# Performance work log

Hardware: AMD Instinct MI355X
Metric: run time of the kernel (lower is better)

Reference implementation:

```python
import jax, jax.numpy as jnp
import numpy as np

B, L, TOPK, NUM_RBF, NUM_POS, MAX_REL, CH = 4, 1024, 30, 16, 16, 32, 128
EDGE_IN = NUM_POS + NUM_RBF * 25 + 18  # 434
NODE_IN = 22


def _normalize(x, axis=-1):
    n = jnp.linalg.norm(x, axis=axis, keepdims=True)
    return jnp.where(n > 0, x / jnp.where(n > 0, n, 1.0), 0.0)


def layer_norm(x, g, b, eps=1e-5):
    mu = jnp.mean(x, axis=-1, keepdims=True)
    var = jnp.var(x, axis=-1, keepdims=True)
    return (x - mu) / jnp.sqrt(var + eps) * g + b


def gather_nodes_d(nodes, idx):
    # nodes [B,M,C], idx [B,N,K] -> [B,N,K,C]
    Bn, N, K = idx.shape
    out = jnp.take_along_axis(nodes, idx.reshape(Bn, N * K, 1), axis=1)
    return out.reshape(Bn, N, K, nodes.shape[-1])


def gather_edges(edges, idx):
    # edges [B,N,N,C], idx [B,N,K] -> [B,N,K,C]
    return jnp.take_along_axis(edges, idx[..., None], axis=2)


def cal_dihedral(Xf, eps=1e-7):
    U = _normalize(Xf[:, 1:, :] - Xf[:, :-1, :])
    u_0, u_1, u_2 = U[:, :-2], U[:, 1:-1], U[:, 2:]
    n_0 = _normalize(jnp.cross(u_0, u_1))
    n_1 = _normalize(jnp.cross(u_1, u_2))
    cosD = jnp.clip(jnp.sum(n_0 * n_1, -1), -1 + eps, 1 - eps)
    v = _normalize(jnp.cross(n_0, n_1))
    return jnp.sign(jnp.sum(-v * u_1, -1)) * jnp.arccos(cosD)


def _dihedrals(X, eps=1e-7):
    Bn, N = X.shape[0], X.shape[1]
    Xf = X[:, :, :3, :].reshape(Bn, 3 * N, 3)
    D = jnp.pad(cal_dihedral(Xf), ((0, 0), (1, 2))).reshape(Bn, N, 3)
    dihedral_feats = jnp.concatenate([jnp.cos(D), jnp.sin(D)], -1)
    U = _normalize(Xf[:, 1:, :] - Xf[:, :-1, :])
    cosA = jnp.clip(jnp.sum(U[:, :-2] * U[:, 1:-1], -1), -1 + eps, 1 - eps)
    A = jnp.pad(jnp.arccos(cosA), ((0, 0), (1, 2))).reshape(Bn, N, 3)
    angle_feats = jnp.concatenate([jnp.cos(A), jnp.sin(A)], -1)
    return jnp.concatenate([dihedral_feats, angle_feats], -1)  # [B,N,12]


def _quaternions(R):
    diag = jnp.diagonal(R, axis1=-2, axis2=-1)
    Rxx, Ryy, Rzz = diag[..., 0], diag[..., 1], diag[..., 2]
    mags = 0.5 * jnp.sqrt(jnp.abs(1.0 + jnp.stack([Rxx - Ryy - Rzz, -Rxx + Ryy - Rzz, -Rxx - Ryy + Rzz], -1)))
    signs = jnp.sign(jnp.stack([R[..., 2, 1] - R[..., 1, 2], R[..., 0, 2] - R[..., 2, 0], R[..., 1, 0] - R[..., 0, 1]], -1))
    w = jnp.sqrt(jax.nn.relu(1.0 + jnp.sum(diag, -1, keepdims=True))) / 2.0
    return _normalize(jnp.concatenate([signs * mags, w], -1))


def _orientations_coarse_gl_tuple(X, E_idx):
    V = X  # [B,N,4,3]
    Bn, N = X.shape[0], X.shape[1]
    Xf = X[:, :, :3, :].reshape(Bn, 3 * N, 3)
    U = _normalize(Xf[:, 1:, :] - Xf[:, :-1, :])
    u_0, u_1 = U[:, :-2], U[:, 1:-1]
    n_0 = _normalize(jnp.cross(u_0, u_1))[:, ::3]  # [B,N-1,3]
    b_1 = _normalize(u_0 - u_1)[:, ::3]
    Xa = Xf[:, ::3]  # N-atom coords [B,N,3]
    Q = jnp.stack([b_1, n_0, jnp.cross(b_1, n_0)], 2).reshape(Bn, N - 1, 9)
    Q = jnp.pad(Q, ((0, 0), (0, 1), (0, 0)))  # [B,N,9]
    Qm = Q.reshape(Bn, N, 3, 3)
    Q_neighbors = gather_nodes_d(Q, E_idx).reshape(Bn, N, -1, 3, 3)
    X_nb = gather_nodes_d(V[:, :, 1, :], E_idx)
    N_nb = gather_nodes_d(V[:, :, 0, :], E_idx)
    C_nb = gather_nodes_d(V[:, :, 2, :], E_idx)
    O_nb = gather_nodes_d(V[:, :, 3, :], E_idx)
    dXn = jnp.stack([X_nb, N_nb, C_nb, O_nb], 3) - Xa[:, :, None, None, :]  # [B,N,K,4,3]
    dU = jnp.einsum('bnij,bnkaj->bnkai', Qm, dXn)
    Kn = E_idx.shape[-1]
    E_direct = _normalize(dU).reshape(Bn, N, Kn, 12)
    R = jnp.einsum('bnji,bnkjl->bnkil', Qm, Q_neighbors)
    q = _quaternions(R)  # [B,N,K,4]
    dX_inner = V[:, :, jnp.array([0, 2, 3]), :] - Xa[:, :, None, :]
    V_direct = _normalize(jnp.einsum('bnij,bnaj->bnai', Qm, dX_inner)).reshape(Bn, N, 9)
    return V_direct, E_direct, q


def _dist(Xc, mask, eps=1e-6):
    mask_2D = mask[:, None, :] * mask[:, :, None]
    D = mask_2D * jnp.sqrt(jnp.sum((Xc[:, None, :, :] - Xc[:, :, None, :]) ** 2, -1) + eps)
    D_max = jnp.max(D, -1, keepdims=True)
    D_adjust = D + (1.0 - mask_2D) * D_max
    negD, E_idx = jax.lax.top_k(-D_adjust, min(TOPK, Xc.shape[1]))
    return -negD, E_idx


def _dist_seq(res_idx):
    D = jnp.abs(res_idx[:, :, None] - res_idx[:, None, :])
    _, E_idx = jax.lax.top_k(-D, min(TOPK, res_idx.shape[1]))
    return E_idx


def _rbf(D):
    D_mu = jnp.linspace(2.0, 22.0, NUM_RBF)
    D_sigma = (22.0 - 2.0) / NUM_RBF
    return jnp.exp(-(((D[..., None] - D_mu) / D_sigma) ** 2))


def _get_rbf(A, Bm, E_idx):
    D = jnp.sqrt(jnp.sum((A[:, :, None, :] - Bm[:, None, :, :]) ** 2, -1) + 1e-6)
    return _rbf(gather_edges(D[..., None], E_idx)[..., 0])


PAIRS = [('N', 'N'), ('C', 'C'), ('O', 'O'), ('Cb', 'Cb'), ('Ca', 'N'), ('Ca', 'C'), ('Ca', 'O'), ('Ca', 'Cb'),
         ('N', 'C'), ('N', 'O'), ('N', 'Cb'), ('Cb', 'C'), ('Cb', 'O'), ('O', 'C'), ('N', 'Ca'), ('C', 'Ca'),
         ('O', 'Ca'), ('Cb', 'Ca'), ('C', 'N'), ('O', 'N'), ('Cb', 'N'), ('C', 'Cb'), ('O', 'Cb'), ('C', 'O')]


def _forward(X, mask, residue_idx, chain_labels, W_pos, b_pos, W_edge, W_node, g_edge, b_edge, g_node, b_node):
    bvec = X[:, :, 1, :] - X[:, :, 0, :]
    cvec = X[:, :, 2, :] - X[:, :, 1, :]
    avec = jnp.cross(bvec, cvec)
    Cb = -0.58273431 * avec + 0.56802827 * bvec - 0.54067466 * cvec + X[:, :, 1, :]
    atoms = {'N': X[:, :, 0, :], 'Ca': X[:, :, 1, :], 'C': X[:, :, 2, :], 'O': X[:, :, 3, :], 'Cb': Cb}
    D_neighbors, E_idx = _dist(atoms['Ca'], mask)
    E_idx_res = _dist_seq(residue_idx)
    E_idx = jnp.where(mask[:, :, None] == 0, E_idx_res, E_idx)
    RBF_all = [_rbf(D_neighbors)]
    for pa, pb in PAIRS:
        RBF_all.append(_get_rbf(atoms[pa], atoms[pb], E_idx))
    RBF_all = jnp.concatenate(RBF_all, -1)  # [B,L,K,400]
    V_angles = _dihedrals(X) * mask[..., None]
    V_direct, E_direct, E_angles = _orientations_coarse_gl_tuple(X, E_idx)
    V_direct = V_direct * mask[..., None]
    offset = residue_idx[:, :, None] - residue_idx[:, None, :]
    E_offset = gather_edges(offset[..., None], E_idx)[..., 0]
    d_chains = (chain_labels[:, :, None] == chain_labels[:, None, :]).astype(jnp.int32)
    E_chains = gather_edges(d_chains[..., None], E_idx)[..., 0]
    d = jnp.clip(E_offset + MAX_REL, 0, 2 * MAX_REL) * E_chains + (1 - E_chains) * (2 * MAX_REL + 1)
    E_positional = jax.nn.one_hot(d, 2 * MAX_REL + 2, dtype=W_pos.dtype) @ W_pos + b_pos
    mask_j = gather_nodes_d(mask[..., None], E_idx)[..., 0]
    fdt = E_direct.dtype
    E = jnp.concatenate([E_positional, RBF_all, E_direct, E_angles,
                         E_chains[..., None].astype(fdt), mask_j[..., None]], -1)  # [B,L,K,434]
    E = layer_norm(E @ W_edge, g_edge, b_edge)
    Vn = jnp.concatenate([V_angles, V_direct, mask[..., None]], -1)  # [B,L,22]
    Vn = layer_norm(Vn @ W_node, g_node, b_node)
    return Vn, E, E_idx


def setup_inputs():
    key = jax.random.key(0)
    ks = jax.random.split(key, 8)
    X = 3.0 * jax.random.normal(ks[0], (B, L, 4, 3), jnp.float32)
    mask = jnp.ones((B, L), jnp.float32)
    residue_idx = jnp.tile(jnp.arange(L, dtype=jnp.int32), (B, 1))
    chain_labels = jax.random.randint(ks[1], (B, L), 0, 2, dtype=jnp.int32)
    s = lambda k, sh: jax.random.normal(k, sh, jnp.float32) * 0.05
    W_pos = s(ks[2], (2 * MAX_REL + 2, NUM_POS))
    b_pos = jnp.zeros((NUM_POS,), jnp.float32)
    W_edge = s(ks[3], (EDGE_IN, CH))
    W_node = s(ks[4], (NODE_IN, CH))
    return dict(X=X, mask=mask, residue_idx=residue_idx, chain_labels=chain_labels,
                W_pos=W_pos, b_pos=b_pos, W_edge=W_edge, W_node=W_node,
                g_edge=jnp.ones((CH,), jnp.float32), b_edge=jnp.zeros((CH,), jnp.float32),
                g_node=jnp.ones((CH,), jnp.float32), b_node=jnp.zeros((CH,), jnp.float32))


def reference(X, mask, residue_idx, chain_labels, W_pos, b_pos, W_edge, W_node, g_edge, b_edge, g_node, b_node):
    return _forward(X, mask, residue_idx, chain_labels, W_pos, b_pos, W_edge, W_node,
                    g_edge, b_edge, g_node, b_node)
```

## Files before the change

kernel.cpp:

```cpp
#include <hip/hip_runtime.h>

#define BATCH 4
#define LEN   1024
#define KNB   30
#define CH    128
#define EIN   434
#define KP    448
#define KST   14
#define ASTR  456
#define CSTR  132
#define AJS   20

typedef unsigned short ushort_t;
typedef __attribute__((ext_vector_type(8))) short bf16x8;
typedef __attribute__((ext_vector_type(4))) float f32x4;

__constant__ int c_pa[24] = {0,2,3,4,1,1,1,1,0,0,0,4,4,3,0,2,3,4,2,3,4,2,3,2};
__constant__ int c_pb[24] = {0,2,3,4,0,2,3,4,2,3,4,2,3,2,1,1,1,1,0,0,0,4,4,3};

struct F3 { float x, y, z; };
__device__ __forceinline__ F3 f3sub(F3 a, F3 b){ return {a.x-b.x, a.y-b.y, a.z-b.z}; }
__device__ __forceinline__ F3 f3cross(F3 a, F3 b){
  return {a.y*b.z - a.z*b.y, a.z*b.x - a.x*b.z, a.x*b.y - a.y*b.x};
}
__device__ __forceinline__ float f3dot(F3 a, F3 b){ return a.x*b.x + a.y*b.y + a.z*b.z; }
__device__ __forceinline__ F3 f3norm(F3 a){
  float s2 = f3dot(a,a);
  float inv = (s2 > 0.f) ? __builtin_amdgcn_rsqf(s2) : 0.f;
  return {a.x*inv, a.y*inv, a.z*inv};
}
__device__ __forceinline__ float fsign(float x){ return (x > 0.f) ? 1.f : ((x < 0.f) ? -1.f : 0.f); }
__device__ __forceinline__ float clip1(float c){ return fminf(fmaxf(c, -1.f + 1e-7f), 1.f - 1e-7f); }

__device__ __forceinline__ void dihedral_cs(F3 ua, F3 ub, F3 uc, float& c, float& s){
  F3 n0 = f3norm(f3cross(ua, ub));
  F3 n1 = f3norm(f3cross(ub, uc));
  float cd = clip1(f3dot(n0, n1));
  F3 v = f3norm(f3cross(n0, n1));
  c = cd;
  s = fsign(-f3dot(v, ub)) * sqrtf(1.f - cd*cd);
}

__device__ __forceinline__ ushort_t f2bf(float f){
  unsigned u = __float_as_uint(f);
  unsigned r = u + 0x7FFFu + ((u >> 16) & 1u);
  return (ushort_t)(r >> 16);
}

__device__ __forceinline__ unsigned cvt_pk(float a, float b){
  unsigned r;
  asm("v_cvt_pk_bf16_f32 %0, %1, %2" : "=v"(r) : "v"(a), "v"(b));
  return r;
}

__device__ __forceinline__ int corig(int c){
  if (c < 16 || c >= 416) return c;
  int base = (c < 216) ? 16 : 216;
  int p = (c - base) >> 3, m = (c - base) & 7;
  return 16 + p*16 + m + ((c < 216) ? 0 : 8);
}

#define DPP_MIN_STEP(v, ctrl) do{                                            \
    unsigned t_ = (unsigned)__builtin_amdgcn_update_dpp(                     \
        (int)0xFFFFFFFF, (int)(v), (ctrl), 0xF, 0xF, false);                 \
    (v) = t_ < (v) ? t_ : (v);                                               \
  } while(0)
__device__ __forceinline__ unsigned wave_min_u32(unsigned v){
  DPP_MIN_STEP(v, 0x111);
  DPP_MIN_STEP(v, 0x112);
  DPP_MIN_STEP(v, 0x114);
  DPP_MIN_STEP(v, 0x118);
  DPP_MIN_STEP(v, 0x142);
  DPP_MIN_STEP(v, 0x143);
  return (unsigned)__builtin_amdgcn_readlane((int)v, 63);
}

__global__ __launch_bounds__(256) void prep_kernel(
    const float* __restrict__ X, const float* __restrict__ mask,
    const float* __restrict__ We,
    float* __restrict__ wCb, float* __restrict__ wQ, float* __restrict__ wVn,
    float* __restrict__ wCa, ushort_t* __restrict__ Wfrag)
{
  if (blockIdx.x >= 16){
    int f = (blockIdx.x - 16)*256 + threadIdx.x;
    if (f >= 8*KST*64) return;
    int t = f / (KST*64);
    int s = (f / 64) % KST;
    int l = f & 63;
    int n  = t*16 + (l & 15);
    int k0 = s*32 + (l >> 4)*8;
    ushort_t v[8];
    #pragma unroll
    for (int j = 0; j < 8; ++j){
      int k = k0 + j;
      v[j] = (k < EIN) ? f2bf(We[(size_t)corig(k)*CH + n]) : (ushort_t)0;
    }
    ulong2* dst = (ulong2*)(Wfrag + (size_t)f*8);
    *dst = *(ulong2*)v;
    return;
  }

  int idx = blockIdx.x * 256 + threadIdx.x;
  int n = idx & (LEN - 1);
  const float* p = X + (size_t)idx * 12;
  const float4* p4 = (const float4*)p;
  float4 q0 = p4[0], q1 = p4[1], q2 = p4[2];
  F3 Na = {q0.x, q0.y, q0.z};
  F3 Ca = {q0.w, q1.x, q1.y};
  F3 Cc = {q1.z, q1.w, q2.x};
  F3 Oa = {q2.y, q2.z, q2.w};
  ((float4*)wCa)[idx] = make_float4(Ca.x, Ca.y, Ca.z, 0.f);
  F3 bv = f3sub(Ca, Na);
  F3 cv = f3sub(Cc, Ca);
  F3 av = f3cross(bv, cv);
  ((float4*)wCb)[idx] = make_float4(
    -0.58273431f*av.x + 0.56802827f*bv.x - 0.54067466f*cv.x + Ca.x,
    -0.58273431f*av.y + 0.56802827f*bv.y - 0.54067466f*cv.y + Ca.y,
    -0.58273431f*av.z + 0.56802827f*bv.z - 0.54067466f*cv.z + Ca.z, 0.f);

  F3 u0 = f3norm(bv);
  F3 u1 = f3norm(cv);

  float Q[9];
  if (n < LEN - 1){
    F3 b1 = f3norm(f3sub(u0, u1));
    F3 n0 = f3norm(f3cross(u0, u1));
    F3 r2 = f3cross(b1, n0);
    Q[0]=b1.x; Q[1]=b1.y; Q[2]=b1.z;
    Q[3]=n0.x; Q[4]=n0.y; Q[5]=n0.z;
    Q[6]=r2.x; Q[7]=r2.y; Q[8]=r2.z;
  } else {
    #pragma unroll
    for (int t = 0; t < 9; ++t) Q[t] = 0.f;
  }
  float4* wq4 = (float4*)(wQ + (size_t)idx*12);
  wq4[0] = make_float4(Q[0], Q[1], Q[2], Q[3]);
  wq4[1] = make_float4(Q[4], Q[5], Q[6], Q[7]);
  wq4[2] = make_float4(Q[8], 0.f, 0.f, 0.f);

  float m = mask[idx];
  bool hp = (n > 0), hn = (n < LEN - 1);
  F3 um1 = {0,0,0}, u2 = {0,0,0}, u3 = {0,0,0};
  if (hp){
    const float* pp = p - 12;
    F3 Cp = {pp[6], pp[7], pp[8]};
    um1 = f3norm(f3sub(Na, Cp));
  }
  if (hn){
    const float* pn = p + 12;
    F3 Nn  = {pn[0], pn[1], pn[2]};
    F3 Can = {pn[3], pn[4], pn[5]};
    u2 = f3norm(f3sub(Nn, Cc));
    u3 = f3norm(f3sub(Can, Nn));
  }
  float cD0=1.f,sD0=0.f, cD1=1.f,sD1=0.f, cD2=1.f,sD2=0.f;
  float cA0=1.f,sA0=0.f, cA1=1.f,sA1=0.f, cA2=1.f,sA2=0.f;
  if (hp){
    dihedral_cs(um1, u0, u1, cD0, sD0);
    cA0 = clip1(f3dot(um1, u0)); sA0 = sqrtf(1.f - cA0*cA0);
  }
  if (hn){
    dihedral_cs(u0, u1, u2, cD1, sD1);
    dihedral_cs(u1, u2, u3, cD2, sD2);
    cA1 = clip1(f3dot(u0, u1)); sA1 = sqrtf(1.f - cA1*cA1);
    cA2 = clip1(f3dot(u1, u2)); sA2 = sqrtf(1.f - cA2*cA2);
  }
  float vn[22];
  vn[0] = cD0*m; vn[1] = cD1*m; vn[2]  = cD2*m;
  vn[3] = sD0*m; vn[4] = sD1*m; vn[5]  = sD2*m;
  vn[6] = cA0*m; vn[7] = cA1*m; vn[8]  = cA2*m;
  vn[9] = sA0*m; vn[10]= sA1*m; vn[11] = sA2*m;
  F3 dxs[3];
  dxs[0] = {0.f, 0.f, 0.f};
  dxs[1] = f3sub(Cc, Na);
  dxs[2] = f3sub(Oa, Na);
  #pragma unroll
  for (int a = 0; a < 3; ++a){
    F3 dv = dxs[a];
    F3 du = { Q[0]*dv.x + Q[1]*dv.y + Q[2]*dv.z,
              Q[3]*dv.x + Q[4]*dv.y + Q[5]*dv.z,
              Q[6]*dv.x + Q[7]*dv.y + Q[8]*dv.z };
    F3 dn = f3norm(du);
    vn[12 + a*3 + 0] = dn.x * m;
    vn[12 + a*3 + 1] = dn.y * m;
    vn[12 + a*3 + 2] = dn.z * m;
  }
  vn[21] = m;
  #pragma unroll
  for (int t = 0; t < 22; ++t) wVn[(size_t)idx*22 + t] = vn[t];
}

__global__ __launch_bounds__(256) void topk_kernel(
    const float* __restrict__ wCa, const float* __restrict__ wVn,
    const float* __restrict__ Wn,  const float* __restrict__ gn,
    const float* __restrict__ bn,
    float* __restrict__ wDn, int* __restrict__ wIdx,
    float* __restrict__ outI, float* __restrict__ outV)
{
  int wid = threadIdx.x >> 6, l = threadIdx.x & 63;
  int bi = blockIdx.x*4 + wid;
  int b  = bi >> 10;
  const float4* Ca = (const float4*)wCa;
  float4 ci = Ca[bi];
  const float4* Cb = Ca + (size_t)b * LEN;

  unsigned D[16];
  #pragma unroll
  for (int t = 0; t < 16; ++t){
    int j = l + 64*t;
    float4 cj = Cb[j];
    float dx = ci.x - cj.x, dy = ci.y - cj.y, dz = ci.z - cj.z;
    D[t] = __float_as_uint(sqrtf(dx*dx + dy*dy + dz*dz + 1e-6f));
  }
  unsigned lmin = D[0]; unsigned jmin = (unsigned)l;
  #pragma unroll
  for (int t = 1; t < 16; ++t)
    if (D[t] < lmin){ lmin = D[t]; jmin = (unsigned)(l + 64*t); }

  for (int k = 0; k < KNB; ++k){
    unsigned dmin = wave_min_u32(lmin);
    unsigned long long tie = __ballot(lmin == dmin);
    bool iwin;
    unsigned jw;
    if (__popcll(tie) == 1ull){
      iwin = (lmin == dmin);
      jw = jmin;
    } else {
      unsigned cand = (lmin == dmin) ? jmin : 0xFFFFFFFFu;
      jw = wave_min_u32(cand);
      iwin = (cand == jw);
    }
    if (iwin){
      wIdx[bi*KNB + k] = (int)jw;
      wDn[bi*KNB + k]  = __uint_as_float(dmin);
      outI[bi*KNB + k] = (float)jw;
      int tw = (int)(jw >> 6);
      #pragma unroll
      for (int t = 0; t < 16; ++t) if (t == tw) D[t] = 0xFFFFFFFFu;
      lmin = D[0]; jmin = (unsigned)l;
      #pragma unroll
      for (int t = 1; t < 16; ++t)
        if (D[t] < lmin){ lmin = D[t]; jmin = (unsigned)(l + 64*t); }
    }
  }

  float x0 = 0.f, x1 = 0.f;
  #pragma unroll
  for (int r = 0; r < 22; ++r){
    float vr = wVn[(size_t)bi*22 + r];
    x0 = fmaf(vr, Wn[r*CH + l],      x0);
    x1 = fmaf(vr, Wn[r*CH + l + 64], x1);
  }
  float sum = x0 + x1;
  #pragma unroll
  for (int off = 1; off < 64; off <<= 1) sum += __shfl_xor(sum, off);
  float mu = sum * (1.f/128.f);
  float d0 = x0 - mu, d1 = x1 - mu;
  float vs = d0*d0 + d1*d1;
  #pragma unroll
  for (int off = 1; off < 64; off <<= 1) vs += __shfl_xor(vs, off);
  float inv = 1.f / sqrtf(vs * (1.f/128.f) + 1e-5f);
  outV[(size_t)bi*CH + l]      = d0*inv*gn[l]    + bn[l];
  outV[(size_t)bi*CH + l + 64] = d1*inv*gn[l+64] + bn[l+64];
}

__global__ __launch_bounds__(512) void edge_kernel(
    const float* __restrict__ X, const float* __restrict__ mask,
    const int* __restrict__ resi, const int* __restrict__ chain,
    const float* __restrict__ Wp, const float* __restrict__ bp,
    const float* __restrict__ ge, const float* __restrict__ be,
    const float* __restrict__ wCb, const float* __restrict__ wQ,
    const float* __restrict__ wDn, const int* __restrict__ wIdx,
    const ushort_t* __restrict__ Wfrag,
    float* __restrict__ outE)
{
  __shared__ __align__(16) ushort_t As[32*ASTR];
  __shared__ __align__(16) float sAJ[KNB][AJS];
  __shared__ __align__(16) float sAI[16];
  __shared__ __align__(16) float sQi[12];

  int bi  = blockIdx.x;
  int b   = bi >> 10;
  int tid = threadIdx.x;
  int w   = tid >> 6, l = tid & 63;

  float qj0=0.f,qj1=0.f,qj2=0.f,qj3=0.f,qj4=0.f,qj5=0.f,qj6=0.f,qj7=0.f,qj8=0.f;
  if (w == 0 && l < KNB){
    int j  = wIdx[bi*KNB + l];
    int gj = (b << 10) + j;
    const float4* pj4 = (const float4*)(X + (size_t)gj * 12);
    *(float4*)&sAJ[l][0] = pj4[0];
    *(float4*)&sAJ[l][4] = pj4[1];
    *(float4*)&sAJ[l][8] = pj4[2];
  } else if (w == 1 && l < KNB){
    int j  = wIdx[bi*KNB + l];
    int gj = (b << 10) + j;
    *(float4*)&sAJ[l][12] = ((const float4*)wCb)[gj];
    sAJ[l][15] = wDn[bi*KNB + l];
    sAJ[l][16] = (chain[bi] == chain[gj]) ? 1.f : 0.f;
    sAJ[l][17] = mask[gj];
    sAJ[l][18] = (float)(resi[bi] - resi[gj]);
  } else if (w == 2 && l < KNB){
    int j  = wIdx[bi*KNB + l];
    int gj = (b << 10) + j;
    const float4* q4 = (const float4*)(wQ + (size_t)gj * 12);
    float4 a = q4[0], bq = q4[1], cq = q4[2];
    qj0=a.x; qj1=a.y; qj2=a.z; qj3=a.w;
    qj4=bq.x; qj5=bq.y; qj6=bq.z; qj7=bq.w;
    qj8=cq.x;
  } else if (w == 3 && l == 0){
    const float4* pi4 = (const float4*)(X + (size_t)bi * 12);
    *(float4*)&sAI[0]  = pi4[0];
    *(float4*)&sAI[4]  = pi4[1];
    *(float4*)&sAI[8]  = pi4[2];
    *(float4*)&sAI[12] = ((const float4*)wCb)[bi];
  } else if (w == 3 && l == 1){
    const float4* q4 = (const float4*)(wQ + (size_t)bi * 12);
    *(float4*)&sQi[0] = q4[0];
    *(float4*)&sQi[4] = q4[1];
    *(float4*)&sQi[8] = q4[2];
  }
  for (int e = tid; e < KNB*14; e += 512){
    int r = e / 14, c = EIN + (e % 14);
    As[r*ASTR + c] = 0;
  }
  __syncthreads();

  auto rbf_task = [&](int tau){
    int k = (int)(((unsigned)tau * 5243u) >> 17);
    int p = tau - k*25;
    float d;
    if (p == 0) d = sAJ[k][15];
    else {
      int ai = c_pa[p-1]*3, bj = c_pb[p-1]*3;
      float dx = sAI[ai+0] - sAJ[k][bj+0];
      float dy = sAI[ai+1] - sAJ[k][bj+1];
      float dz = sAI[ai+2] - sAJ[k][bj+2];
      d = sqrtf(dx*dx + dy*dy + dz*dz + 1e-6f);
    }
    float A  = d*d*(-0.92332483f);
    float Bc = d*1.84664966f;
    unsigned u[8];
    #pragma unroll
    for (int h = 0; h < 8; ++h){
      float mu0 = 2.f + (2*h  )*(4.f/3.f);
      float mu1 = 2.f + (2*h+1)*(4.f/3.f);
      float e0 = __builtin_amdgcn_exp2f(fmaf(Bc, mu0, A + (-0.92332483f*mu0*mu0)));
      float e1 = __builtin_amdgcn_exp2f(fmaf(Bc, mu1, A + (-0.92332483f*mu1*mu1)));
      u[h] = cvt_pk(e0, e1);
    }
    *(uint4*)&As[k*ASTR + 16  + p*8] = make_uint4(u[0], u[1], u[2], u[3]);
    *(uint4*)&As[k*ASTR + 216 + p*8] = make_uint4(u[4], u[5], u[6], u[7]);
  };

  rbf_task(tid);
  if (tid >= 274) rbf_task(tid + 238);

  if (w == 1 && l < KNB){
    int k = l;
    ushort_t* row = &As[k*ASTR];
    float ch = sAJ[k][16];
    int off  = (int)sAJ[k][18];
    int dpos = off + 32;
    dpos = dpos < 0 ? 0 : (dpos > 64 ? 64 : dpos);
    if (!(ch > 0.5f)) dpos = 65;
    const float4* wp4 = (const float4*)(Wp + dpos*16);
    const float4* bp4 = (const float4*)bp;
    unsigned u[8];
    #pragma unroll
    for (int h = 0; h < 4; ++h){
      float4 wv = wp4[h], bv = bp4[h];
      u[2*h]   = cvt_pk(wv.x + bv.x, wv.y + bv.y);
      u[2*h+1] = cvt_pk(wv.z + bv.z, wv.w + bv.w);
    }
    *(uint4*)&row[0] = make_uint4(u[0], u[1], u[2], u[3]);
    *(uint4*)&row[8] = make_uint4(u[4], u[5], u[6], u[7]);
    *(unsigned*)&row[432] = cvt_pk(ch, sAJ[k][17]);
  } else if (w == 2 && l < KNB){
    int k = l;
    ushort_t* row = &As[k*ASTR];
    float R[3][3];
    R[0][0] = sQi[0]*qj0 + sQi[3]*qj3 + sQi[6]*qj6;
    R[0][1] = sQi[0]*qj1 + sQi[3]*qj4 + sQi[6]*qj7;
    R[0][2] = sQi[0]*qj2 + sQi[3]*qj5 + sQi[6]*qj8;
    R[1][0] = sQi[1]*qj0 + sQi[4]*qj3 + sQi[7]*qj6;
    R[1][1] = sQi[1]*qj1 + sQi[4]*qj4 + sQi[7]*qj7;
    R[1][2] = sQi[1]*qj2 + sQi[4]*qj5 + sQi[7]*qj8;
    R[2][0] = sQi[2]*qj0 + sQi[5]*qj3 + sQi[8]*qj6;
    R[2][1] = sQi[2]*qj1 + sQi[5]*qj4 + sQi[8]*qj7;
    R[2][2] = sQi[2]*qj2 + sQi[5]*qj5 + sQi[8]*qj8;
    float Rxx = R[0][0], Ryy = R[1][1], Rzz = R[2][2];
    float mx = 0.5f*sqrtf(fabsf(1.f + Rxx - Ryy - Rzz));
    float my = 0.5f*sqrtf(fabsf(1.f - Rxx + Ryy - Rzz));
    float mz = 0.5f*sqrtf(fabsf(1.f - Rxx - Ryy + Rzz));
    float qx = fsign(R[2][1] - R[1][2]) * mx;
    float qy = fsign(R[0][2] - R[2][0]) * my;
    float qz = fsign(R[1][0] - R[0][1]) * mz;
    float qw = sqrtf(fmaxf(1.f + Rxx + Ryy + Rzz, 0.f)) * 0.5f;
    float qn2 = qx*qx + qy*qy + qz*qz + qw*qw;
    float inv = qn2 > 0.f ? __builtin_amdgcn_rsqf(qn2) : 0.f;
    *(uint2*)&row[428] = make_uint2(cvt_pk(qx*inv, qy*inv), cvt_pk(qz*inv, qw*inv));
  } else if (w == 3 && l < KNB){
    int k = l;
    ushort_t* row = &As[k*ASTR];
    float nx = sAI[0], ny = sAI[1], nz = sAI[2];
    const int amap[4] = {3, 0, 6, 9};
    float f[12];
    #pragma unroll
    for (int a = 0; a < 4; ++a){
      float dx = sAJ[k][amap[a]+0] - nx;
      float dy = sAJ[k][amap[a]+1] - ny;
      float dz = sAJ[k][amap[a]+2] - nz;
      float e0 = sQi[0]*dx + sQi[1]*dy + sQi[2]*dz;
      float e1 = sQi[3]*dx + sQi[4]*dy + sQi[5]*dz;
      float e2 = sQi[6]*dx + sQi[7]*dy + sQi[8]*dz;
      float ss = e0*e0 + e1*e1 + e2*e2;
      float inv = ss > 0.f ? __builtin_amdgcn_rsqf(ss) : 0.f;
      f[a*3+0] = e0*inv; f[a*3+1] = e1*inv; f[a*3+2] = e2*inv;
    }
    unsigned u[6];
    #pragma unroll
    for (int h = 0; h < 6; ++h) u[h] = cvt_pk(f[2*h], f[2*h+1]);
    *(uint4*)&row[416] = make_uint4(u[0], u[1], u[2], u[3]);
    *(uint2*)&row[424] = make_uint2(u[4], u[5]);
  }
  __syncthreads();

  int mt = w >> 2, np = w & 3;
  int aOff = mt*16*ASTR + (l & 15)*ASTR + (l >> 4)*8;
  const ushort_t* bpw0 = Wfrag + ((size_t)((2*np  )*KST)*64 + l)*8;
  const ushort_t* bpw1 = Wfrag + ((size_t)((2*np+1)*KST)*64 + l)*8;

  f32x4 acc0 = {0.f,0.f,0.f,0.f}, acc1 = acc0;

  bf16x8 a  = *(const bf16x8*)&As[aOff];
  bf16x8 b0 = *(const bf16x8*)bpw0;
  bf16x8 b1 = *(const bf16x8*)bpw1;
  #pragma unroll
  for (int s = 0; s < KST; ++s){
    bf16x8 an, b0n, b1n;
    if (s < KST-1){
      an  = *(const bf16x8*)&As[aOff + (s+1)*32];
      b0n = *(const bf16x8*)(bpw0 + (size_t)(s+1)*64*8);
      b1n = *(const bf16x8*)(bpw1 + (size_t)(s+1)*64*8);
    }
    acc0 = __builtin_amdgcn_mfma_f32_16x16x32_bf16(a, b0, acc0, 0, 0, 0);
    acc1 = __builtin_amdgcn_mfma_f32_16x16x32_bf16(a, b1, acc1, 0, 0, 0);
    if (s < KST-1){ a = an; b0 = b0n; b1 = b1n; }
  }
  __syncthreads();

  float* Cs = (float*)As;
  int ccol = l & 15, crow = (l >> 4)*4;
  #pragma unroll
  for (int r = 0; r < 4; ++r){
    Cs[(mt*16 + crow + r)*CSTR + np*32      + ccol] = acc0[r];
    Cs[(mt*16 + crow + r)*CSTR + np*32 + 16 + ccol] = acc1[r];
  }
  __syncthreads();

  if (tid < KNB*16){
    int row = tid >> 4, g = tid & 15;
    const float4* vr = (const float4*)&Cs[row*CSTR + g*8];
    float4 v0 = vr[0], v1 = vr[1];
    float v[8] = {v0.x,v0.y,v0.z,v0.w, v1.x,v1.y,v1.z,v1.w};
    float s = 0.f;
    #pragma unroll
    for (int c = 0; c < 8; ++c) s += v[c];
    #pragma unroll
    for (int off = 1; off < 16; off <<= 1) s += __shfl_xor(s, off, 16);
    float mu = s * (1.f/128.f);
    float vs = 0.f;
    #pragma unroll
    for (int c = 0; c < 8; ++c){ float dd = v[c] - mu; vs += dd*dd; }
    #pragma unroll
    for (int off = 1; off < 16; off <<= 1) vs += __shfl_xor(vs, off, 16);
    float inv = 1.f / sqrtf(vs * (1.f/128.f) + 1e-5f);
    const float4* g4 = (const float4*)&ge[g*8];
    const float4* b4 = (const float4*)&be[g*8];
    float4 ga = g4[0], gb = g4[1], ba = b4[0], bb = b4[1];
    float4 o0, o1;
    o0.x = (v[0]-mu)*inv*ga.x + ba.x;  o0.y = (v[1]-mu)*inv*ga.y + ba.y;
    o0.z = (v[2]-mu)*inv*ga.z + ba.z;  o0.w = (v[3]-mu)*inv*ga.w + ba.w;
    o1.x = (v[4]-mu)*inv*gb.x + bb.x;  o1.y = (v[5]-mu)*inv*gb.y + bb.y;
    o1.z = (v[6]-mu)*inv*gb.z + bb.z;  o1.w = (v[7]-mu)*inv*gb.w + bb.w;
    float4* dst = (float4*)&outE[((size_t)bi*KNB + row)*CH + g*8];
    dst[0] = o0;
    dst[1] = o1;
  }
}

extern "C" void kernel_launch(void* const* d_in, const int* in_sizes, int n_in,
                              void* d_out, int out_size, void* d_ws, size_t ws_size,
                              hipStream_t stream)
{
  const float* X    = (const float*)d_in[0];
  const float* mask = (const float*)d_in[1];
  const int*   resi = (const int*)  d_in[2];
  const int*   chn  = (const int*)  d_in[3];
  const float* Wp   = (const float*)d_in[4];
  const float* bp   = (const float*)d_in[5];
  const float* We   = (const float*)d_in[6];
  const float* Wn   = (const float*)d_in[7];
  const float* ge   = (const float*)d_in[8];
  const float* be   = (const float*)d_in[9];
  const float* gn   = (const float*)d_in[10];
  const float* bn   = (const float*)d_in[11];

  float* outV = (float*)d_out;
  float* outE = outV + (size_t)BATCH*LEN*CH;
  float* outI = outE + (size_t)BATCH*LEN*KNB*CH;

  float* ws   = (float*)d_ws;
  float* wCb  = ws;
  float* wQ   = wCb + (size_t)BATCH*LEN*4;
  float* wVn  = wQ  + (size_t)BATCH*LEN*12;
  float* wDn  = wVn + (size_t)BATCH*LEN*22;
  int*   wIdx = (int*)(wDn + (size_t)BATCH*LEN*KNB);
  float* wCa  = (float*)(wIdx + (size_t)BATCH*LEN*KNB);
  ushort_t* Wfrag = (ushort_t*)(wCa + (size_t)BATCH*LEN*4);

  prep_kernel<<<16 + 28, 256, 0, stream>>>(X, mask, We, wCb, wQ, wVn, wCa, Wfrag);
  topk_kernel<<<BATCH*LEN/4, 256, 0, stream>>>(wCa, wVn, Wn, gn, bn,
                                               wDn, wIdx, outI, outV);
  edge_kernel<<<BATCH*LEN, 512, 0, stream>>>(X, mask, resi, chn, Wp, bp, ge, be,
                                             wCb, wQ, wDn, wIdx, Wfrag, outE);
}
```

Baseline: 165.8 us.

## Prefetch weight fragments at kernel start and remap waves to column tiles

Each wave now owns one 16-column N tile across both 16-row M tiles, instead of one M tile and two N tiles. This halves the global weight-fragment loads per wave. The first half of the wave's B fragments is loaded into registers at kernel entry so the loads overlap the feature-construction phase, and the rest is streamed inside the MFMA loop. The launch bounds also gain a minimum-blocks hint. The cost is more register pressure from holding 14 bf16x8 fragments plus a second A fragment, which could cause spills, especially under the occupancy hint.

```diff
diff --git a/kernel.cpp b/kernel.cpp
--- a/kernel.cpp
+++ b/kernel.cpp
@@ -10,6 +10,7 @@
 #define ASTR  456
 #define CSTR  132
 #define AJS   20
+#define BPF   7
 
 typedef unsigned short ushort_t;
 typedef __attribute__((ext_vector_type(8))) short bf16x8;
@@ -264,7 +265,7 @@
   outV[(size_t)bi*CH + l + 64] = d1*inv*gn[l+64] + bn[l+64];
 }
 
-__global__ __launch_bounds__(512) void edge_kernel(
+__global__ __launch_bounds__(512, 8) void edge_kernel(
     const float* __restrict__ X, const float* __restrict__ mask,
     const int* __restrict__ resi, const int* __restrict__ chain,
     const float* __restrict__ Wp, const float* __restrict__ bp,
@@ -283,6 +284,12 @@
   int b   = bi >> 10;
   int tid = threadIdx.x;
   int w   = tid >> 6, l = tid & 63;
+
+  const ushort_t* bpw = Wfrag + ((size_t)(w*KST)*64 + l)*8;
+  bf16x8 bq[KST];
+  #pragma unroll
+  for (int s = 0; s < BPF; ++s)
+    bq[s] = *(const bf16x8*)(bpw + (size_t)s*64*8);
 
   float qj0=0.f,qj1=0.f,qj2=0.f,qj3=0.f,qj4=0.f,qj5=0.f,qj6=0.f,qj7=0.f,qj8=0.f;
   if (w == 0 && l < KNB){
@@ -304,9 +311,9 @@
     int j  = wIdx[bi*KNB + l];
     int gj = (b << 10) + j;
     const float4* q4 = (const float4*)(wQ + (size_t)gj * 12);
-    float4 a = q4[0], bq = q4[1], cq = q4[2];
+    float4 a = q4[0], bq2 = q4[1], cq = q4[2];
     qj0=a.x; qj1=a.y; qj2=a.z; qj3=a.w;
-    qj4=bq.x; qj5=bq.y; qj6=bq.z; qj7=bq.w;
+    qj4=bq2.x; qj5=bq2.y; qj6=bq2.z; qj7=bq2.w;
     qj8=cq.x;
   } else if (w == 3 && l == 0){
     const float4* pi4 = (const float4*)(X + (size_t)bi * 12);
@@ -426,27 +433,26 @@
   }
   __syncthreads();
 
-  int mt = w >> 2, np = w & 3;
-  int aOff = mt*16*ASTR + (l & 15)*ASTR + (l >> 4)*8;
-  const ushort_t* bpw0 = Wfrag + ((size_t)((2*np  )*KST)*64 + l)*8;
-  const ushort_t* bpw1 = Wfrag + ((size_t)((2*np+1)*KST)*64 + l)*8;
+  int aOff0 = (l & 15)*ASTR + (l >> 4)*8;
+  int aOff1 = aOff0 + 16*ASTR;
 
   f32x4 acc0 = {0.f,0.f,0.f,0.f}, acc1 = acc0;
 
-  bf16x8 a  = *(const bf16x8*)&As[aOff];
-  bf16x8 b0 = *(const bf16x8*)bpw0;
-  bf16x8 b1 = *(const bf16x8*)bpw1;
+  bf16x8 a0 = *(const bf16x8*)&As[aOff0];
+  bf16x8 a1 = *(const bf16x8*)&As[aOff1];
   #pragma unroll
   for (int s = 0; s < KST; ++s){
-    bf16x8 an, b0n, b1n;
+    if (s + BPF < KST)
+      bq[s + BPF] = *(const bf16x8*)(bpw + (size_t)(s + BPF)*64*8);
+    bf16x8 a0n, a1n;
     if (s < KST-1){
-      an  = *(const bf16x8*)&As[aOff + (s+1)*32];
-      b0n = *(const bf16x8*)(bpw0 + (size_t)(s+1)*64*8);
-      b1n = *(const bf16x8*)(bpw1 + (size_t)(s+1)*64*8);
-    }
-    acc0 = __builtin_amdgcn_mfma_f32_16x16x32_bf16(a, b0, acc0, 0, 0, 0);
-    acc1 = __builtin_amdgcn_mfma_f32_16x16x32_bf16(a, b1, acc1, 0, 0, 0);
-    if (s < KST-1){ a = an; b0 = b0n; b1 = b1n; }
+      int ka = (s+1)*32;
+      a0n = *(const bf16x8*)&As[aOff0 + ka];
+      a1n = *(const bf16x8*)&As[aOff1 + ka];
+    }
+    acc0 = __builtin_amdgcn_mfma_f32_16x16x32_bf16(a0, bq[s], acc0, 0, 0, 0);
+    acc1 = __builtin_amdgcn_mfma_f32_16x16x32_bf16(a1, bq[s], acc1, 0, 0, 0);
+    if (s < KST-1){ a0 = a0n; a1 = a1n; }
   }
   __syncthreads();
 
@@ -454,8 +460,8 @@
   int ccol = l & 15, crow = (l >> 4)*4;
   #pragma unroll
   for (int r = 0; r < 4; ++r){
-    Cs[(mt*16 + crow + r)*CSTR + np*32      + ccol] = acc0[r];
-    Cs[(mt*16 + crow + r)*CSTR + np*32 + 16 + ccol] = acc1[r];
+    Cs[(crow + r)*CSTR      + w*16 + ccol] = acc0[r];
+    Cs[(16 + crow + r)*CSTR + w*16 + ccol] = acc1[r];
   }
   __syncthreads();
 
```

After: 177.2 us. 6.9% more time.
